# Kernel tuning notes

Measured on AMD Instinct MI355X. Metric: run time of the kernel, lower is better.

Reference implementation:

```python
import jax, jax.numpy as jnp
import numpy as np

D_K = 64
NEG_INF = -1.0e9

def setup_inputs() -> dict:
    key = jax.random.key(0)
    kq, kk, kv, km = jax.random.split(key, 4)
    B, H, S, D = 2, 16, 2048, D_K
    Q = jax.random.normal(kq, (B, H, S, D), dtype=jnp.float32)
    K = jax.random.normal(kk, (B, H, S, D), dtype=jnp.float32)
    V = jax.random.normal(kv, (B, H, S, D), dtype=jnp.float32)
    # True entries are masked out (torch masked_fill semantics)
    attn_mask = jax.random.randint(km, (B, H, S, S), 0, 2).astype(jnp.bool_)
    return {"Q": Q, "K": K, "V": V, "attn_mask": attn_mask}

def reference(Q, K, V, attn_mask):
    # scores: [B, H, len_q, len_k]
    scale = 1.0 / np.sqrt(D_K).astype(np.float32)
    scores = jnp.einsum('bhqd,bhkd->bhqk', Q, K) * scale
    scores = jnp.where(attn_mask, jnp.float32(NEG_INF), scores)
    attn = jax.nn.softmax(scores, axis=-1)
    prob = jnp.einsum('bhqk,bhkd->bhqd', attn, V)
    return (prob, attn)
```

## Files before the change

### kernel.cpp

```cpp
#include <hip/hip_runtime.h>
#include <hip/hip_bf16.h>

#define S_LEN 2048
#define D_DIM 64
#define QT    64
#define KT    64
#define NTHR  256
#define NKT   (S_LEN / KT)
#define NBLK  1024
#define PROB_ELEMS 4194304LL

typedef float        f32x4  __attribute__((ext_vector_type(4)));
typedef int          i32x4  __attribute__((ext_vector_type(4)));
typedef unsigned int u32x4  __attribute__((ext_vector_type(4)));
typedef short        bf16x8 __attribute__((ext_vector_type(8)));

__device__ __forceinline__ unsigned short f2bf(float f) {
    return __builtin_bit_cast(unsigned short, __float2bfloat16(f));
}
__device__ __forceinline__ int swzc(int row, int ch) {
    return ch ^ ((row ^ (row >> 3)) & 7);
}
__device__ __forceinline__ float4 scale4(float4 v, float s) {
    v.x *= s; v.y *= s; v.z *= s; v.w *= s; return v;
}
__device__ __forceinline__ u32x4 packbf(float4 a, float4 b) {
    u32x4 r;
    r[0] = (unsigned)f2bf(a.x) | ((unsigned)f2bf(a.y) << 16);
    r[1] = (unsigned)f2bf(a.z) | ((unsigned)f2bf(a.w) << 16);
    r[2] = (unsigned)f2bf(b.x) | ((unsigned)f2bf(b.y) << 16);
    r[3] = (unsigned)f2bf(b.z) | ((unsigned)f2bf(b.w) << 16);
    return r;
}
__device__ __forceinline__ unsigned cvtpk(float lo, float hi) {
    unsigned r;
    asm("v_cvt_pk_bf16_f32 %0, %1, %2" : "=v"(r) : "v"(lo), "v"(hi));
    return r;
}
__device__ __forceinline__ void glds16(const unsigned* g, unsigned char* l) {
    __builtin_amdgcn_global_load_lds(
        (const __attribute__((address_space(1))) unsigned*)g,
        (__attribute__((address_space(3))) unsigned*)(void*)l, 16, 0, 0);
}

__global__ void mask_probe_kernel(const unsigned int* __restrict__ m,
                                  int* __restrict__ flag) {
    unsigned int v = m[threadIdx.x];
    unsigned long long ok = __ballot(v <= 1u);
    if (threadIdx.x == 0) *flag = (ok == ~0ULL) ? 1 : 0;
}

#define KPART 524288
#define VPART 65536
__global__ __launch_bounds__(256)
void kv_prep(const float* __restrict__ Kg, const float* __restrict__ Vg,
             unsigned* __restrict__ Kbf, unsigned* __restrict__ Vtb) {
    int tid = blockIdx.x * 256 + threadIdx.x;
    if (tid < KPART) {
        int ch = tid & 7, rowg = tid >> 3;
        const float* src = Kg + (long long)rowg * D_DIM + ch * 8;
        float4 a = *(const float4*)src, b = *(const float4*)(src + 4);
        int bh = rowg >> 11, k = rowg & 2047, kt = k >> 6, row = k & 63;
        unsigned* dst = Kbf + ((unsigned)(bh * NKT + kt) << 11)
                            + row * 32 + swzc(row, ch) * 4;
        *(u32x4*)dst = packbf(a, b);
    } else if (tid < KPART + VPART) {
        int idx = tid - KPART;
        int d = idx & 63, kt = (idx >> 6) & 31, bh = idx >> 11;
        const float* vb = Vg + (long long)(bh * S_LEN + kt * KT) * D_DIM + d;
        unsigned* tile = Vtb + ((unsigned)(bh * NKT + kt) << 11) + d * 32;
        #pragma unroll
        for (int ci = 0; ci < 8; ++ci) {
            u32x4 o;
            #pragma unroll
            for (int s = 0; s < 4; ++s) {
                float lo = vb[(ci * 8 + 2 * s) * D_DIM];
                float hi = vb[(ci * 8 + 2 * s + 1) * D_DIM];
                o[s] = (unsigned)f2bf(lo) | ((unsigned)f2bf(hi) << 16);
            }
            *(u32x4*)(tile + swzc(d, ci) * 4) = o;
        }
    }
}


#define LOAD_MBITS(DST, KTV)                                                \
    { unsigned bz = 0u;                                                     \
      _Pragma("unroll")                                                     \
      for (int n = 0; n < 4; ++n) {                                         \
        unsigned idx = rowoff + (unsigned)((KTV) * KT + n * 16 + 4 * g);    \
        if (mask32) {                                                       \
            i32x4 m4 = *(const i32x4*)(((const int*)maskB) + idx);          \
            bz |= ((m4[0] ? 1u : 0u) | (m4[1] ? 2u : 0u) |                  \
                   (m4[2] ? 4u : 0u) | (m4[3] ? 8u : 0u)) << (n * 4);       \
        } else {                                                            \
            unsigned mb = *(const unsigned*)(maskB + idx);                  \
            bz |= (((mb & 0xffu) ? 1u : 0u) | ((mb & 0xff00u) ? 2u : 0u) |  \
                   ((mb & 0xff0000u) ? 4u : 0u) |                           \
                   ((mb & 0xff000000u) ? 8u : 0u)) << (n * 4);              \
        } }                                                                 \
      (DST) = bz; }

#define LOAD_BITS2(DST, KTV)                                                \
    { if (useWS) (DST) = (unsigned)bitsWS[bitbase + (unsigned)(KTV) * NTHR];\
      else LOAD_MBITS(DST, KTV) }

#define PH1_TILE(KS, BITS)                                                  \
    { unsigned bb = (BITS);                                                 \
      _Pragma("unroll")                                                     \
      for (int n = 0; n < 4; ++n) {                                         \
        int rowk = n * 16 + c;                                              \
        bf16x8 kf0 = *(const bf16x8*)((KS) + rowk * 128 + swzc(rowk, g) * 16);     \
        bf16x8 kf1 = *(const bf16x8*)((KS) + rowk * 128 + swzc(rowk, 4 + g) * 16); \
        f32x4 acc = {0.f, 0.f, 0.f, 0.f};                                   \
        acc = __builtin_amdgcn_mfma_f32_16x16x32_bf16(kf0, qf0, acc, 0, 0, 0); \
        acc = __builtin_amdgcn_mfma_f32_16x16x32_bf16(kf1, qf1, acc, 0, 0, 0); \
        unsigned mb = bb >> (n * 4);                                        \
        psum += (mb & 1u) ? 0.f : __expf(acc[0]);                           \
        psum += (mb & 2u) ? 0.f : __expf(acc[1]);                           \
        psum += (mb & 4u) ? 0.f : __expf(acc[2]);                           \
        psum += (mb & 8u) ? 0.f : __expf(acc[3]);                           \
      } }

#define PH2_TILE(KS, VT, BITS, KTV)                                         \
    { unsigned bb = (BITS);                                                 \
      _Pragma("unroll")                                                     \
      for (int n = 0; n < 4; ++n) {                                         \
        int rowk = n * 16 + c;                                              \
        bf16x8 kf0 = *(const bf16x8*)((KS) + rowk * 128 + swzc(rowk, g) * 16);     \
        bf16x8 kf1 = *(const bf16x8*)((KS) + rowk * 128 + swzc(rowk, 4 + g) * 16); \
        f32x4 acc = {0.f, 0.f, 0.f, 0.f};                                   \
        acc = __builtin_amdgcn_mfma_f32_16x16x32_bf16(kf0, qf0, acc, 0, 0, 0); \
        acc = __builtin_amdgcn_mfma_f32_16x16x32_bf16(kf1, qf1, acc, 0, 0, 0); \
        unsigned mb = bb >> (n * 4);                                        \
        f32x4 ev;                                                           \
        ev[0] = (mb & 1u) ? 0.f : __expf(acc[0]) * rinv;                    \
        ev[1] = (mb & 2u) ? 0.f : __expf(acc[1]) * rinv;                    \
        ev[2] = (mb & 4u) ? 0.f : __expf(acc[2]) * rinv;                    \
        ev[3] = (mb & 8u) ? 0.f : __expf(acc[3]) * rinv;                    \
        unsigned idx0 = rowoff + (unsigned)((KTV) * KT + n * 16 + 4 * g);   \
        __builtin_nontemporal_store(ev, (f32x4*)(attnOut + idx0));          \
        uint2 pkv; pkv.x = cvtpk(ev[0], ev[1]); pkv.y = cvtpk(ev[2], ev[3]);\
        int kloc = n * 16 + 4 * g;                                          \
        *(uint2*)(Ps + ql * 128 + swzc(ql, kloc >> 3) * 16 + (kloc & 7) * 2) = pkv; \
      }                                                                     \
      { bf16x8 pa0 = *(const bf16x8*)(Ps + ql * 128 + swzc(ql, g) * 16);    \
        bf16x8 pa1 = *(const bf16x8*)(Ps + ql * 128 + swzc(ql, 4 + g) * 16);\
        __builtin_amdgcn_s_setprio(1);                                      \
        _Pragma("unroll")                                                   \
        for (int df = 0; df < 4; ++df) {                                    \
            int d = df * 16 + c;                                            \
            bf16x8 vb0 = *(const bf16x8*)((VT) + d * 128 + swzc(d, g) * 16);     \
            bf16x8 vb1 = *(const bf16x8*)((VT) + d * 128 + swzc(d, 4 + g) * 16); \
            pacc[df] = __builtin_amdgcn_mfma_f32_16x16x32_bf16(pa0, vb0, pacc[df], 0, 0, 0); \
            pacc[df] = __builtin_amdgcn_mfma_f32_16x16x32_bf16(pa1, vb1, pacc[df], 0, 0, 0); \
        }                                                                   \
        __builtin_amdgcn_s_setprio(0); } }

__global__ __launch_bounds__(NTHR, 4)
void attn_fused_glds(const float* __restrict__ Qg,
                     const unsigned* __restrict__ Kbf,
                     const unsigned* __restrict__ Vtb,
                     const unsigned char* __restrict__ maskB,
                     const int* __restrict__ flagp,
                     unsigned short* __restrict__ bitsWS, int useWS,
                     float* __restrict__ attnOut, float* __restrict__ probOut) {
    __shared__ unsigned char sm[40960];
    unsigned char* Ks0 = sm;
    unsigned char* Ks1 = sm + 8192;
    unsigned char* Vt0 = sm + 16384;
    unsigned char* Vt1 = sm + 24576;
    unsigned char* Ps  = sm + 32768;

    const int t = threadIdx.x;
    const int lane = t & 63, w = t >> 6, c = lane & 15, g = lane >> 4;

    const int orig = blockIdx.x;
    const int virt = (orig & 7) * 128 + (orig >> 3);
    const int qt = virt & 31, bh = virt >> 5;
    const int mask32 = *flagp;

    const int qrowbase = bh * S_LEN + qt * QT;
    const int ql = w * 16 + c;
    const unsigned rowoff = (unsigned)(qrowbase + ql) * (unsigned)S_LEN;
    const unsigned bitbase = (unsigned)virt * NKT * NTHR + (unsigned)t;
    const unsigned ktile0 = (unsigned)(bh * NKT) << 11;

    const int f0u = t * 4, f1u = (NTHR + t) * 4;
    const int dst0 = (t & ~63) * 16, dst1 = (NTHR + (t & ~63)) * 16;

    #pragma unroll
    for (int i = 0; i < 2; ++i) {
        int flat = i * NTHR + t, row = flat >> 3, ch = flat & 7;
        const float* src = Qg + (qrowbase + row) * D_DIM + ch * 8;
        float4 a = *(const float4*)src, b = *(const float4*)(src + 4);
        *(u32x4*)(Ps + row * 128 + swzc(row, ch) * 16) =
            packbf(scale4(a, 0.125f), scale4(b, 0.125f));
    }
    __syncthreads();
    bf16x8 qf0 = *(const bf16x8*)(Ps + ql * 128 + swzc(ql, g) * 16);
    bf16x8 qf1 = *(const bf16x8*)(Ps + ql * 128 + swzc(ql, 4 + g) * 16);

    float psum = 0.f;
    unsigned bA, bB;
    {
        const unsigned* kp = Kbf + ktile0;
        glds16(kp + f0u, Ks0 + dst0);
        glds16(kp + f1u, Ks0 + dst1);
    }
    LOAD_MBITS(bA, 0)

    for (int j = 0; j < NKT / 2; ++j) {
        const int ktA = 2 * j, ktB = 2 * j + 1;
        __syncthreads();
        {
            const unsigned* kp = Kbf + ktile0 + (unsigned)ktB * 2048;
            glds16(kp + f0u, Ks1 + dst0);
            glds16(kp + f1u, Ks1 + dst1);
        }
        LOAD_MBITS(bB, ktB)
        PH1_TILE(Ks0, bA)
        if (useWS) bitsWS[bitbase + (unsigned)ktA * NTHR] = (unsigned short)bA;

        __syncthreads();
        if (j + 1 < NKT / 2) {
            const unsigned* kp = Kbf + ktile0 + (unsigned)(ktA + 2) * 2048;
            glds16(kp + f0u, Ks0 + dst0);
            glds16(kp + f1u, Ks0 + dst1);
            LOAD_MBITS(bA, ktA + 2)
        }
        PH1_TILE(Ks1, bB)
        if (useWS) bitsWS[bitbase + (unsigned)ktB * NTHR] = (unsigned short)bB;
    }

    float s = psum;
    s += __shfl_xor(s, 16, 64);
    s += __shfl_xor(s, 32, 64);
    const float rinv = 1.0f / s;

    f32x4 pacc[4];
    #pragma unroll
    for (int d = 0; d < 4; ++d) pacc[d] = (f32x4){0.f, 0.f, 0.f, 0.f};

    {
        const unsigned* kp = Kbf + ktile0;
        const unsigned* vp = Vtb + ktile0;
        glds16(kp + f0u, Ks0 + dst0); glds16(kp + f1u, Ks0 + dst1);
        glds16(vp + f0u, Vt0 + dst0); glds16(vp + f1u, Vt0 + dst1);
    }
    LOAD_BITS2(bA, 0)

    for (int j = 0; j < NKT / 2; ++j) {
        const int ktA = 2 * j, ktB = 2 * j + 1;
        __syncthreads();
        {
            const unsigned* kp = Kbf + ktile0 + (unsigned)ktB * 2048;
            const unsigned* vp = Vtb + ktile0 + (unsigned)ktB * 2048;
            glds16(kp + f0u, Ks1 + dst0); glds16(kp + f1u, Ks1 + dst1);
            glds16(vp + f0u, Vt1 + dst0); glds16(vp + f1u, Vt1 + dst1);
        }
        LOAD_BITS2(bB, ktB)
        PH2_TILE(Ks0, Vt0, bA, ktA)

        __syncthreads();
        if (j + 1 < NKT / 2) {
            const unsigned* kp = Kbf + ktile0 + (unsigned)(ktA + 2) * 2048;
            const unsigned* vp = Vtb + ktile0 + (unsigned)(ktA + 2) * 2048;
            glds16(kp + f0u, Ks0 + dst0); glds16(kp + f1u, Ks0 + dst1);
            glds16(vp + f0u, Vt0 + dst0); glds16(vp + f1u, Vt0 + dst1);
            LOAD_BITS2(bA, ktA + 2)
        }
        PH2_TILE(Ks1, Vt1, bB, ktB)
    }

    #pragma unroll
    for (int df = 0; df < 4; ++df)
        #pragma unroll
        for (int r = 0; r < 4; ++r) {
            int qe = w * 16 + g * 4 + r;
            probOut[(long long)(qrowbase + qe) * D_DIM + df * 16 + c] = pacc[df][r];
        }
}

#define LOAD_K(KP, KTV)                                                     \
    { _Pragma("unroll")                                                     \
      for (int i = 0; i < 2; ++i) {                                         \
        int flat = i * NTHR + t, row = flat >> 3, ch = flat & 7;            \
        const float* src = Kg + (kbase + (KTV) * KT + row) * D_DIM + ch * 8;\
        float4 a = *(const float4*)src, b = *(const float4*)(src + 4);      \
        KP[i] = packbf(a, b);                                               \
      } }
#define STAGE_K(KS, KP)                                                     \
    { _Pragma("unroll")                                                     \
      for (int i = 0; i < 2; ++i) {                                         \
        int flat = i * NTHR + t, row = flat >> 3, ch = flat & 7;            \
        *(u32x4*)((KS) + row * 128 + swzc(row, ch) * 16) = KP[i];           \
      } }
#define LOAD_V(VP, KTV)                                                     \
    { const float* src = Vg + (kbase + (KTV) * KT + k0v) * D_DIM + dgv * 8; \
      float4 a = *(const float4*)src, b = *(const float4*)(src + 4);        \
      float4 e4 = *(const float4*)(src + D_DIM);                            \
      float4 f4 = *(const float4*)(src + D_DIM + 4);                        \
      VP[0] = (unsigned)f2bf(a.x) | ((unsigned)f2bf(e4.x) << 16);           \
      VP[1] = (unsigned)f2bf(a.y) | ((unsigned)f2bf(e4.y) << 16);           \
      VP[2] = (unsigned)f2bf(a.z) | ((unsigned)f2bf(e4.z) << 16);           \
      VP[3] = (unsigned)f2bf(a.w) | ((unsigned)f2bf(e4.w) << 16);           \
      VP[4] = (unsigned)f2bf(b.x) | ((unsigned)f2bf(f4.x) << 16);           \
      VP[5] = (unsigned)f2bf(b.y) | ((unsigned)f2bf(f4.y) << 16);           \
      VP[6] = (unsigned)f2bf(b.z) | ((unsigned)f2bf(f4.z) << 16);           \
      VP[7] = (unsigned)f2bf(b.w) | ((unsigned)f2bf(f4.w) << 16); }
#define STAGE_V(VT, VP)                                                     \
    { _Pragma("unroll")                                                     \
      for (int jj = 0; jj < 8; ++jj) {                                      \
        int d = dgv * 8 + jj;                                               \
        *(unsigned*)((VT) + d * 128 + swzc(d, k0v >> 3) * 16 + (k0v & 7) * 2) = VP[jj]; \
      } }

__global__ __launch_bounds__(NTHR, 4)
void attn_fused_reg(const float* __restrict__ Qg, const float* __restrict__ Kg,
                    const float* __restrict__ Vg,
                    const unsigned char* __restrict__ maskB,
                    const int* __restrict__ flagp,
                    unsigned short* __restrict__ bitsWS, int useWS,
                    float* __restrict__ attnOut, float* __restrict__ probOut) {
    __shared__ unsigned char sm[40960];
    unsigned char* Ks0 = sm;
    unsigned char* Ks1 = sm + 8192;
    unsigned char* Vt0 = sm + 16384;
    unsigned char* Vt1 = sm + 24576;
    unsigned char* Ps  = sm + 32768;

    const int t = threadIdx.x;
    const int lane = t & 63, w = t >> 6, c = lane & 15, g = lane >> 4;

    const int orig = blockIdx.x;
    const int virt = (orig & 7) * 128 + (orig >> 3);
    const int qt = virt & 31, bh = virt >> 5;
    const int mask32 = *flagp;

    const int qrowbase = bh * S_LEN + qt * QT;
    const int kbase = bh * S_LEN;
    const int ql = w * 16 + c;
    const unsigned rowoff = (unsigned)(qrowbase + ql) * (unsigned)S_LEN;
    const unsigned bitbase = (unsigned)virt * NKT * NTHR + (unsigned)t;
    const int dgv = t & 7, k0v = (t >> 3) * 2;

    #pragma unroll
    for (int i = 0; i < 2; ++i) {
        int flat = i * NTHR + t, row = flat >> 3, ch = flat & 7;
        const float* src = Qg + (qrowbase + row) * D_DIM + ch * 8;
        float4 a = *(const float4*)src, b = *(const float4*)(src + 4);
        *(u32x4*)(Ps + row * 128 + swzc(row, ch) * 16) =
            packbf(scale4(a, 0.125f), scale4(b, 0.125f));
    }
    __syncthreads();
    bf16x8 qf0 = *(const bf16x8*)(Ps + ql * 128 + swzc(ql, g) * 16);
    bf16x8 qf1 = *(const bf16x8*)(Ps + ql * 128 + swzc(ql, 4 + g) * 16);
    __syncthreads();

    float psum = 0.f;
    u32x4 kpA[2], kpB[2];
    unsigned bA, bB;
    LOAD_K(kpA, 0)
    LOAD_MBITS(bA, 0)

    for (int j = 0; j < NKT / 2; ++j) {
        const int ktA = 2 * j, ktB = 2 * j + 1;
        STAGE_K(Ks0, kpA)
        LOAD_K(kpB, ktB)
        LOAD_MBITS(bB, ktB)
        __syncthreads();
        PH1_TILE(Ks0, bA)
        if (useWS) bitsWS[bitbase + (unsigned)ktA * NTHR] = (unsigned short)bA;
        STAGE_K(Ks1, kpB)
        if (j + 1 < NKT / 2) {
            LOAD_K(kpA, ktA + 2)
            LOAD_MBITS(bA, ktA + 2)
        }
        __syncthreads();
        PH1_TILE(Ks1, bB)
        if (useWS) bitsWS[bitbase + (unsigned)ktB * NTHR] = (unsigned short)bB;
    }

    float s = psum;
    s += __shfl_xor(s, 16, 64);
    s += __shfl_xor(s, 32, 64);
    const float rinv = 1.0f / s;

    f32x4 pacc[4];
    #pragma unroll
    for (int d = 0; d < 4; ++d) pacc[d] = (f32x4){0.f, 0.f, 0.f, 0.f};

    unsigned vpA[8], vpB[8];
    LOAD_K(kpA, 0)
    LOAD_V(vpA, 0)
    LOAD_BITS2(bA, 0)
    __syncthreads();

    for (int j = 0; j < NKT / 2; ++j) {
        const int ktA = 2 * j, ktB = 2 * j + 1;
        STAGE_K(Ks0, kpA)
        STAGE_V(Vt0, vpA)
        LOAD_K(kpB, ktB)
        LOAD_V(vpB, ktB)
        LOAD_BITS2(bB, ktB)
        __syncthreads();
        PH2_TILE(Ks0, Vt0, bA, ktA)
        STAGE_K(Ks1, kpB)
        STAGE_V(Vt1, vpB)
        if (j + 1 < NKT / 2) {
            LOAD_K(kpA, ktA + 2)
            LOAD_V(vpA, ktA + 2)
            LOAD_BITS2(bA, ktA + 2)
        }
        __syncthreads();
        PH2_TILE(Ks1, Vt1, bB, ktB)
    }

    #pragma unroll
    for (int df = 0; df < 4; ++df)
        #pragma unroll
        for (int r = 0; r < 4; ++r) {
            int qe = w * 16 + g * 4 + r;
            probOut[(long long)(qrowbase + qe) * D_DIM + df * 16 + c] = pacc[df][r];
        }
}

extern "C" void kernel_launch(void* const* d_in, const int* in_sizes, int n_in,
                              void* d_out, int out_size, void* d_ws, size_t ws_size,
                              hipStream_t stream) {
    const float* Q = (const float*)d_in[0];
    const float* K = (const float*)d_in[1];
    const float* V = (const float*)d_in[2];
    const unsigned char* mask = (const unsigned char*)d_in[3];

    float* prob = (float*)d_out;
    float* attn = (float*)d_out + PROB_ELEMS;

    const size_t bits_bytes = (size_t)NBLK * NKT * NTHR * 2ull;
    const size_t kbf_bytes  = 8388608ull;
    int* flag = (int*)d_ws;
    unsigned short* bitsWS = (unsigned short*)((char*)d_ws + 256);
    unsigned* Kbf = (unsigned*)((char*)d_ws + 256 + bits_bytes);
    unsigned* Vtb = (unsigned*)((char*)d_ws + 256 + bits_bytes + kbf_bytes);

    const int useWS   = (ws_size >= 256 + bits_bytes) ? 1 : 0;
    const int usePrep = (ws_size >= 256 + bits_bytes + 2 * kbf_bytes) ? 1 : 0;

    mask_probe_kernel<<<1, 64, 0, stream>>>((const unsigned int*)mask, flag);
    if (usePrep) {
        kv_prep<<<(KPART + VPART) / 256, 256, 0, stream>>>(K, V, Kbf, Vtb);
        attn_fused_glds<<<NBLK, NTHR, 0, stream>>>(Q, Kbf, Vtb, mask, flag,
                                                   bitsWS, useWS, attn, prob);
    } else {
        attn_fused_reg<<<NBLK, NTHR, 0, stream>>>(Q, K, V, mask, flag,
                                                  bitsWS, useWS, attn, prob);
    }
}
```

Before: 365.3 us.

## Replace syncthreads with vmcnt-counted barriers and prefetch mask ahead in glds kernel

The global-to-LDS kernel's double-buffered loops now use explicit s_waitcnt vmcnt(N) plus s_barrier with scheduling fences instead of __syncthreads. This lets in-flight K/V loads for the next tile stay outstanding while the current tile computes. Raw mask loads are issued a tile ahead into registers and converted to bits later, which hides mask latency behind MFMA work. The attn output store changes from nontemporal to a regular store. The vmcnt counts are hand-tuned, so any mismatch with the actual number of outstanding loads would be a correctness hazard.

Result: no change. 367.1 us (+0.5%).

```diff
diff --git a/kernel.cpp b/kernel.cpp
--- a/kernel.cpp
+++ b/kernel.cpp
@@ -42,6 +42,16 @@
         (const __attribute__((address_space(1))) unsigned*)g,
         (__attribute__((address_space(3))) unsigned*)(void*)l, 16, 0, 0);
 }
+#define BC8(x) __builtin_bit_cast(bf16x8, (x))
+#define MFMA(A, B, C) __builtin_amdgcn_mfma_f32_16x16x32_bf16((A), (B), (C), 0, 0, 0)
+
+#define SFENCE() __builtin_amdgcn_sched_barrier(0)
+#define WAITBAR(N)                                                          \
+    SFENCE();                                                               \
+    asm volatile("s_waitcnt vmcnt(" #N ")" ::: "memory");                   \
+    SFENCE();                                                               \
+    __builtin_amdgcn_s_barrier();                                           \
+    SFENCE();
 
 __global__ void mask_probe_kernel(const unsigned int* __restrict__ m,
                                   int* __restrict__ flag) {
@@ -83,29 +93,46 @@
     }
 }
 
-
-#define LOAD_MBITS(DST, KTV)                                                \
-    { unsigned bz = 0u;                                                     \
-      _Pragma("unroll")                                                     \
-      for (int n = 0; n < 4; ++n) {                                         \
-        unsigned idx = rowoff + (unsigned)((KTV) * KT + n * 16 + 4 * g);    \
-        if (mask32) {                                                       \
-            i32x4 m4 = *(const i32x4*)(((const int*)maskB) + idx);          \
-            bz |= ((m4[0] ? 1u : 0u) | (m4[1] ? 2u : 0u) |                  \
-                   (m4[2] ? 4u : 0u) | (m4[3] ? 8u : 0u)) << (n * 4);       \
-        } else {                                                            \
-            unsigned mb = *(const unsigned*)(maskB + idx);                  \
-            bz |= (((mb & 0xffu) ? 1u : 0u) | ((mb & 0xff00u) ? 2u : 0u) |  \
-                   ((mb & 0xff0000u) ? 4u : 0u) |                           \
-                   ((mb & 0xff000000u) ? 8u : 0u)) << (n * 4);              \
-        } }                                                                 \
-      (DST) = bz; }
-
-#define LOAD_BITS2(DST, KTV)                                                \
-    { if (useWS) (DST) = (unsigned)bitsWS[bitbase + (unsigned)(KTV) * NTHR];\
-      else LOAD_MBITS(DST, KTV) }
-
-#define PH1_TILE(KS, BITS)                                                  \
+#define GLDS_K(KS, KTV)                                                     \
+    { const unsigned* kp_ = Kbf + ktile0 + (unsigned)(KTV) * 2048u;         \
+      glds16(kp_ + f0u, (KS) + dst0); glds16(kp_ + f1u, (KS) + dst1); }
+#define GLDS_V(VT, KTV)                                                     \
+    { const unsigned* vp_ = Vtb + ktile0 + (unsigned)(KTV) * 2048u;         \
+      glds16(vp_ + f0u, (VT) + dst0); glds16(vp_ + f1u, (VT) + dst1); }
+
+#define PREF_MASKF(MI4, MU, KTV)                                            \
+    { if (mask32) {                                                         \
+        _Pragma("unroll")                                                   \
+        for (int n_ = 0; n_ < 4; ++n_)                                      \
+          MI4[n_] = *(const i32x4*)(maskI + rowoff                          \
+                      + (unsigned)((KTV) * KT + n_ * 16 + 4 * g));          \
+      } else {                                                              \
+        _Pragma("unroll")                                                   \
+        for (int n_ = 0; n_ < 4; ++n_)                                      \
+          MU[n_] = *(const unsigned*)(maskB + rowoff                        \
+                      + (unsigned)((KTV) * KT + n_ * 16 + 4 * g));          \
+      } }
+
+#define BITS16F(DST, MI4, MU)                                               \
+    { unsigned bz_ = 0u;                                                    \
+      if (mask32) {                                                         \
+        _Pragma("unroll")                                                   \
+        for (int n_ = 0; n_ < 4; ++n_)                                      \
+          bz_ |= ((MI4[n_][0] ? 1u : 0u) | (MI4[n_][1] ? 2u : 0u) |         \
+                  (MI4[n_][2] ? 4u : 0u) | (MI4[n_][3] ? 8u : 0u)) << (n_ * 4); \
+      } else {                                                              \
+        _Pragma("unroll")                                                   \
+        for (int n_ = 0; n_ < 4; ++n_) { unsigned mb_ = MU[n_];             \
+          bz_ |= (((mb_ & 0xffu) ? 1u : 0u) | ((mb_ & 0xff00u) ? 2u : 0u) | \
+                  ((mb_ & 0xff0000u) ? 4u : 0u) |                           \
+                  ((mb_ & 0xff000000u) ? 8u : 0u)) << (n_ * 4); }           \
+      }                                                                     \
+      (DST) = bz_; }
+
+#define GLOAD_BITS(DST, KTV)                                                \
+    { (DST) = (unsigned)bitsWS[bitbase + (unsigned)(KTV) * NTHR]; }
+
+#define GP1_TILE(KS, BITS)                                                  \
     { unsigned bb = (BITS);                                                 \
       _Pragma("unroll")                                                     \
       for (int n = 0; n < 4; ++n) {                                         \
@@ -113,8 +140,7 @@
         bf16x8 kf0 = *(const bf16x8*)((KS) + rowk * 128 + swzc(rowk, g) * 16);     \
         bf16x8 kf1 = *(const bf16x8*)((KS) + rowk * 128 + swzc(rowk, 4 + g) * 16); \
         f32x4 acc = {0.f, 0.f, 0.f, 0.f};                                   \
-        acc = __builtin_amdgcn_mfma_f32_16x16x32_bf16(kf0, qf0, acc, 0, 0, 0); \
-        acc = __builtin_amdgcn_mfma_f32_16x16x32_bf16(kf1, qf1, acc, 0, 0, 0); \
+        acc = MFMA(kf0, qf0, acc); acc = MFMA(kf1, qf1, acc);               \
         unsigned mb = bb >> (n * 4);                                        \
         psum += (mb & 1u) ? 0.f : __expf(acc[0]);                           \
         psum += (mb & 2u) ? 0.f : __expf(acc[1]);                           \
@@ -122,7 +148,7 @@
         psum += (mb & 8u) ? 0.f : __expf(acc[3]);                           \
       } }
 
-#define PH2_TILE(KS, VT, BITS, KTV)                                         \
+#define GP2_TILE(KS, VT, BITS, KTV)                                         \
     { unsigned bb = (BITS);                                                 \
       _Pragma("unroll")                                                     \
       for (int n = 0; n < 4; ++n) {                                         \
@@ -130,8 +156,7 @@
         bf16x8 kf0 = *(const bf16x8*)((KS) + rowk * 128 + swzc(rowk, g) * 16);     \
         bf16x8 kf1 = *(const bf16x8*)((KS) + rowk * 128 + swzc(rowk, 4 + g) * 16); \
         f32x4 acc = {0.f, 0.f, 0.f, 0.f};                                   \
-        acc = __builtin_amdgcn_mfma_f32_16x16x32_bf16(kf0, qf0, acc, 0, 0, 0); \
-        acc = __builtin_amdgcn_mfma_f32_16x16x32_bf16(kf1, qf1, acc, 0, 0, 0); \
+        acc = MFMA(kf0, qf0, acc); acc = MFMA(kf1, qf1, acc);               \
         unsigned mb = bb >> (n * 4);                                        \
         f32x4 ev;                                                           \
         ev[0] = (mb & 1u) ? 0.f : __expf(acc[0]) * rinv;                    \
@@ -139,7 +164,7 @@
         ev[2] = (mb & 4u) ? 0.f : __expf(acc[2]) * rinv;                    \
         ev[3] = (mb & 8u) ? 0.f : __expf(acc[3]) * rinv;                    \
         unsigned idx0 = rowoff + (unsigned)((KTV) * KT + n * 16 + 4 * g);   \
-        __builtin_nontemporal_store(ev, (f32x4*)(attnOut + idx0));          \
+        *(f32x4*)(attnOut + idx0) = ev;              \
         uint2 pkv; pkv.x = cvtpk(ev[0], ev[1]); pkv.y = cvtpk(ev[2], ev[3]);\
         int kloc = n * 16 + 4 * g;                                          \
         *(uint2*)(Ps + ql * 128 + swzc(ql, kloc >> 3) * 16 + (kloc & 7) * 2) = pkv; \
@@ -152,8 +177,8 @@
             int d = df * 16 + c;                                            \
             bf16x8 vb0 = *(const bf16x8*)((VT) + d * 128 + swzc(d, g) * 16);     \
             bf16x8 vb1 = *(const bf16x8*)((VT) + d * 128 + swzc(d, 4 + g) * 16); \
-            pacc[df] = __builtin_amdgcn_mfma_f32_16x16x32_bf16(pa0, vb0, pacc[df], 0, 0, 0); \
-            pacc[df] = __builtin_amdgcn_mfma_f32_16x16x32_bf16(pa1, vb1, pacc[df], 0, 0, 0); \
+            pacc[df] = MFMA(pa0, vb0, pacc[df]);                            \
+            pacc[df] = MFMA(pa1, vb1, pacc[df]);                            \
         }                                                                   \
         __builtin_amdgcn_s_setprio(0); } }
 
@@ -174,11 +199,13 @@
 
     const int t = threadIdx.x;
     const int lane = t & 63, w = t >> 6, c = lane & 15, g = lane >> 4;
+    (void)lane;
 
     const int orig = blockIdx.x;
     const int virt = (orig & 7) * 128 + (orig >> 3);
     const int qt = virt & 31, bh = virt >> 5;
     const int mask32 = *flagp;
+    const int* maskI = (const int*)maskB;
 
     const int qrowbase = bh * S_LEN + qt * QT;
     const int ql = w * 16 + c;
@@ -202,37 +229,36 @@
     bf16x8 qf1 = *(const bf16x8*)(Ps + ql * 128 + swzc(ql, 4 + g) * 16);
 
     float psum = 0.f;
-    unsigned bA, bB;
     {
-        const unsigned* kp = Kbf + ktile0;
-        glds16(kp + f0u, Ks0 + dst0);
-        glds16(kp + f1u, Ks0 + dst1);
-    }
-    LOAD_MBITS(bA, 0)
-
-    for (int j = 0; j < NKT / 2; ++j) {
-        const int ktA = 2 * j, ktB = 2 * j + 1;
-        __syncthreads();
-        {
-            const unsigned* kp = Kbf + ktile0 + (unsigned)ktB * 2048;
-            glds16(kp + f0u, Ks1 + dst0);
-            glds16(kp + f1u, Ks1 + dst1);
-        }
-        LOAD_MBITS(bB, ktB)
-        PH1_TILE(Ks0, bA)
-        if (useWS) bitsWS[bitbase + (unsigned)ktA * NTHR] = (unsigned short)bA;
-
-        __syncthreads();
-        if (j + 1 < NKT / 2) {
-            const unsigned* kp = Kbf + ktile0 + (unsigned)(ktA + 2) * 2048;
-            glds16(kp + f0u, Ks0 + dst0);
-            glds16(kp + f1u, Ks0 + dst1);
-            LOAD_MBITS(bA, ktA + 2)
-        }
-        PH1_TILE(Ks1, bB)
-        if (useWS) bitsWS[bitbase + (unsigned)ktB * NTHR] = (unsigned short)bB;
-    }
-
+        unsigned bA, bB;
+        i32x4 mAi[4], mBi[4];
+        unsigned mAu[4], mBu[4];
+
+        GLDS_K(Ks0, 0)
+        PREF_MASKF(mAi, mAu, 0)
+        WAITBAR(0)
+
+        for (int j = 0; j < NKT / 2; ++j) {
+            const int ktA = 2 * j, ktB = 2 * j + 1;
+            GLDS_K(Ks1, ktB)
+            PREF_MASKF(mBi, mBu, ktB)
+            SFENCE();
+            BITS16F(bA, mAi, mAu)
+            GP1_TILE(Ks0, bA)
+            if (useWS) bitsWS[bitbase + (unsigned)ktA * NTHR] = (unsigned short)bA;
+            WAITBAR(1)
+
+            if (j + 1 < NKT / 2) {
+                GLDS_K(Ks0, ktA + 2)
+                PREF_MASKF(mAi, mAu, ktA + 2)
+            }
+            SFENCE();
+            BITS16F(bB, mBi, mBu)
+            GP1_TILE(Ks1, bB)
+            if (useWS) bitsWS[bitbase + (unsigned)ktB * NTHR] = (unsigned short)bB;
+            WAITBAR(1)
+        }
+    }
     float s = psum;
     s += __shfl_xor(s, 16, 64);
     s += __shfl_xor(s, 32, 64);
@@ -241,36 +267,28 @@
     f32x4 pacc[4];
     #pragma unroll
     for (int d = 0; d < 4; ++d) pacc[d] = (f32x4){0.f, 0.f, 0.f, 0.f};
-
     {
-        const unsigned* kp = Kbf + ktile0;
-        const unsigned* vp = Vtb + ktile0;
-        glds16(kp + f0u, Ks0 + dst0); glds16(kp + f1u, Ks0 + dst1);
-        glds16(vp + f0u, Vt0 + dst0); glds16(vp + f1u, Vt0 + dst1);
-    }
-    LOAD_BITS2(bA, 0)
-
-    for (int j = 0; j < NKT / 2; ++j) {
-        const int ktA = 2 * j, ktB = 2 * j + 1;
-        __syncthreads();
-        {
-            const unsigned* kp = Kbf + ktile0 + (unsigned)ktB * 2048;
-            const unsigned* vp = Vtb + ktile0 + (unsigned)ktB * 2048;
-            glds16(kp + f0u, Ks1 + dst0); glds16(kp + f1u, Ks1 + dst1);
-            glds16(vp + f0u, Vt1 + dst0); glds16(vp + f1u, Vt1 + dst1);
-        }
-        LOAD_BITS2(bB, ktB)
-        PH2_TILE(Ks0, Vt0, bA, ktA)
-
-        __syncthreads();
-        if (j + 1 < NKT / 2) {
-            const unsigned* kp = Kbf + ktile0 + (unsigned)(ktA + 2) * 2048;
-            const unsigned* vp = Vtb + ktile0 + (unsigned)(ktA + 2) * 2048;
-            glds16(kp + f0u, Ks0 + dst0); glds16(kp + f1u, Ks0 + dst1);
-            glds16(vp + f0u, Vt0 + dst0); glds16(vp + f1u, Vt0 + dst1);
-            LOAD_BITS2(bA, ktA + 2)
-        }
-        PH2_TILE(Ks1, Vt1, bB, ktB)
+        unsigned bA, bB;
+        GLDS_K(Ks0, 0) GLDS_V(Vt0, 0)
+        GLOAD_BITS(bA, 0)
+        WAITBAR(0)
+
+        for (int j = 0; j < NKT / 2; ++j) {
+            const int ktA = 2 * j, ktB = 2 * j + 1;
+            GLDS_K(Ks1, ktB) GLDS_V(Vt1, ktB)
+            GLOAD_BITS(bB, ktB)
+            SFENCE();
+            GP2_TILE(Ks0, Vt0, bA, ktA)
+            WAITBAR(4)
+
+            if (j + 1 < NKT / 2) {
+                GLDS_K(Ks0, ktA + 2) GLDS_V(Vt0, ktA + 2)
+                GLOAD_BITS(bA, ktA + 2)
+            }
+            SFENCE();
+            GP2_TILE(Ks1, Vt1, bB, ktB)
+            WAITBAR(4)
+        }
     }
 
     #pragma unroll
@@ -282,7 +300,28 @@
         }
 }
 
-#define LOAD_K(KP, KTV)                                                     \
+#define FB_MBITS(DST, KTV)                                                  \
+    { unsigned bz_ = 0u;                                                    \
+      _Pragma("unroll")                                                     \
+      for (int n_ = 0; n_ < 4; ++n_) {                                      \
+        unsigned idx_ = rowoff + (unsigned)((KTV) * KT + n_ * 16 + 4 * g);  \
+        if (mask32) {                                                       \
+            i32x4 m4_ = *(const i32x4*)(maskI + idx_);                      \
+            bz_ |= ((m4_[0] ? 1u : 0u) | (m4_[1] ? 2u : 0u) |               \
+                    (m4_[2] ? 4u : 0u) | (m4_[3] ? 8u : 0u)) << (n_ * 4);   \
+        } else {                                                            \
+            unsigned mb_ = *(const unsigned*)(maskB + idx_);                \
+            bz_ |= (((mb_ & 0xffu) ? 1u : 0u) | ((mb_ & 0xff00u) ? 2u : 0u) | \
+                    ((mb_ & 0xff0000u) ? 4u : 0u) |                         \
+                    ((mb_ & 0xff000000u) ? 8u : 0u)) << (n_ * 4);           \
+        } }                                                                 \
+      (DST) = bz_; }
+
+#define FB_BITS2(DST, KTV)                                                  \
+    { if (useWS) (DST) = (unsigned)bitsWS[bitbase + (unsigned)(KTV)*NTHR];  \
+      else FB_MBITS(DST, KTV) }
+
+#define FB_LOAD_K(KP, KTV)                                                  \
     { _Pragma("unroll")                                                     \
       for (int i = 0; i < 2; ++i) {                                         \
         int flat = i * NTHR + t, row = flat >> 3, ch = flat & 7;            \
@@ -290,13 +329,13 @@
         float4 a = *(const float4*)src, b = *(const float4*)(src + 4);      \
         KP[i] = packbf(a, b);                                               \
       } }
-#define STAGE_K(KS, KP)                                                     \
+#define FB_STAGE_K(KS, KP)                                                  \
     { _Pragma("unroll")                                                     \
       for (int i = 0; i < 2; ++i) {                                         \
         int flat = i * NTHR + t, row = flat >> 3, ch = flat & 7;            \
         *(u32x4*)((KS) + row * 128 + swzc(row, ch) * 16) = KP[i];           \
       } }
-#define LOAD_V(VP, KTV)                                                     \
+#define FB_LOAD_V(VP, KTV)                                                  \
     { const float* src = Vg + (kbase + (KTV) * KT + k0v) * D_DIM + dgv * 8; \
       float4 a = *(const float4*)src, b = *(const float4*)(src + 4);        \
       float4 e4 = *(const float4*)(src + D_DIM);                            \
@@ -309,7 +348,7 @@
       VP[5] = (unsigned)f2bf(b.y) | ((unsigned)f2bf(f4.y) << 16);           \
       VP[6] = (unsigned)f2bf(b.z) | ((unsigned)f2bf(f4.z) << 16);           \
       VP[7] = (unsigned)f2bf(b.w) | ((unsigned)f2bf(f4.w) << 16); }
-#define STAGE_V(VT, VP)                                                     \
+#define FB_STAGE_V(VT, VP)                                                  \
     { _Pragma("unroll")                                                     \
       for (int jj = 0; jj < 8; ++jj) {                                      \
         int d = dgv * 8 + jj;                                               \
@@ -332,11 +371,13 @@
 
     const int t = threadIdx.x;
     const int lane = t & 63, w = t >> 6, c = lane & 15, g = lane >> 4;
+    (void)lane;
 
     const int orig = blockIdx.x;
     const int virt = (orig & 7) * 128 + (orig >> 3);
     const int qt = virt & 31, bh = virt >> 5;
     const int mask32 = *flagp;
+    const int* maskI = (const int*)maskB;
 
     const int qrowbase = bh * S_LEN + qt * QT;
     const int kbase = bh * S_LEN;
@@ -361,24 +402,24 @@
     float psum = 0.f;
     u32x4 kpA[2], kpB[2];
     unsigned bA, bB;
-    LOAD_K(kpA, 0)
-    LOAD_MBITS(bA, 0)
+    FB_LOAD_K(kpA, 0)
+    FB_MBITS(bA, 0)
 
     for (int j = 0; j < NKT / 2; ++j) {
         const int ktA = 2 * j, ktB = 2 * j + 1;
-        STAGE_K(Ks0, kpA)
-        LOAD_K(kpB, ktB)
-        LOAD_MBITS(bB, ktB)
+        FB_STAGE_K(Ks0, kpA)
+        FB_LOAD_K(kpB, ktB)
+        FB_MBITS(bB, ktB)
         __syncthreads();
-        PH1_TILE(Ks0, bA)
+        GP1_TILE(Ks0, bA)
         if (useWS) bitsWS[bitbase + (unsigned)ktA * NTHR] = (unsigned short)bA;
-        STAGE_K(Ks1, kpB)
+        FB_STAGE_K(Ks1, kpB)
         if (j + 1 < NKT / 2) {
-            LOAD_K(kpA, ktA + 2)
-            LOAD_MBITS(bA, ktA + 2)
+            FB_LOAD_K(kpA, ktA + 2)
+            FB_MBITS(bA, ktA + 2)
         }
         __syncthreads();
-        PH1_TILE(Ks1, bB)
+        GP1_TILE(Ks1, bB)
         if (useWS) bitsWS[bitbase + (unsigned)ktB * NTHR] = (unsigned short)bB;
     }
 
@@ -392,29 +433,29 @@
     for (int d = 0; d < 4; ++d) pacc[d] = (f32x4){0.f, 0.f, 0.f, 0.f};
 
     unsigned vpA[8], vpB[8];
-    LOAD_K(kpA, 0)
-    LOAD_V(vpA, 0)
-    LOAD_BITS2(bA, 0)
+    FB_LOAD_K(kpA, 0)
+    FB_LOAD_V(vpA, 0)
+    FB_BITS2(bA, 0)
     __syncthreads();
 
     for (int j = 0; j < NKT / 2; ++j) {
         const int ktA = 2 * j, ktB = 2 * j + 1;
-        STAGE_K(Ks0, kpA)
-        STAGE_V(Vt0, vpA)
-        LOAD_K(kpB, ktB)
-        LOAD_V(vpB, ktB)
-        LOAD_BITS2(bB, ktB)
+        FB_STAGE_K(Ks0, kpA)
+        FB_STAGE_V(Vt0, vpA)
+        FB_LOAD_K(kpB, ktB)
+        FB_LOAD_V(vpB, ktB)
+        FB_BITS2(bB, ktB)
         __syncthreads();
-        PH2_TILE(Ks0, Vt0, bA, ktA)
-        STAGE_K(Ks1, kpB)
-        STAGE_V(Vt1, vpB)
+        GP2_TILE(Ks0, Vt0, bA, ktA)
+        FB_STAGE_K(Ks1, kpB)
+        FB_STAGE_V(Vt1, vpB)
         if (j + 1 < NKT / 2) {
-            LOAD_K(kpA, ktA + 2)
-            LOAD_V(vpA, ktA + 2)
-            LOAD_BITS2(bA, ktA + 2)
+            FB_LOAD_K(kpA, ktA + 2)
+            FB_LOAD_V(vpA, ktA + 2)
+            FB_BITS2(bA, ktA + 2)
         }
         __syncthreads();
-        PH2_TILE(Ks1, Vt1, bB, ktB)
+        GP2_TILE(Ks1, Vt1, bB, ktB)
     }
 
     #pragma unroll
@@ -448,7 +489,7 @@
     const int usePrep = (ws_size >= 256 + bits_bytes + 2 * kbf_bytes) ? 1 : 0;
 
     mask_probe_kernel<<<1, 64, 0, stream>>>((const unsigned int*)mask, flag);
-    if (usePrep) {
+    if (usePrep && useWS) {
         kv_prep<<<(KPART + VPART) / 256, 256, 0, stream>>>(K, V, Kbf, Vtb);
         attn_fused_glds<<<NBLK, NTHR, 0, stream>>>(Q, Kbf, Vtb, mask, flag,
                                                    bitsWS, useWS, attn, prob);
```
